# Performance work log

Hardware: AMD Instinct MI355X
Metric: run time of the kernel (lower is better)

## Reference

```python
import jax, jax.numpy as jnp
import numpy as np

NU, NI, ED, H = 30000, 10000, 64, 4
D = ED * H            # fusion_dim = 256
N = NU + NI           # total graph nodes
E = 100000            # edges
B = 8192              # scored (user, wine) pairs
NST, SD = 4, 64       # side tokens / side token dim
NEG = -1e30


def setup_inputs():
    key = jax.random.key(0)
    ks = iter(jax.random.split(key, 64))

    def w(*shape):
        return jax.random.normal(next(ks), shape, jnp.float32) * 0.05

    return {
        "user": jax.random.randint(next(ks), (B,), 0, NU),
        "wine": jax.random.randint(next(ks), (B,), 0, NI),
        "edge_index": jax.random.randint(next(ks), (2, E), 0, N),
        "keep_edge": jax.random.uniform(next(ks), (E,)) > 0.2,   # edge_dropout keep mask
        "node_mask": jax.random.uniform(next(ks), (N,)) < 0.2,   # mask-autoencoding mask
        "user_emb": w(NU, ED),
        "wine_emb": w(NI, ED),
        "up_w": w(ED, D), "up_b": w(D),
        "wp_w": w(ED, D), "wp_b": w(D),
        "sf_proj_w": w(SD, D), "sf_proj_b": w(D),
        "sf_q_w": w(D, D), "sf_q_b": w(D),
        "sf_k_w": w(D, D), "sf_k_b": w(D),
        "sf_v_w": w(D, D), "sf_v_b": w(D),
        "sf_o_w": w(D, D), "sf_o_b": w(D),
        "sf_fc_w": w(2 * D, D), "sf_fc_b": w(D),
        "g_w": w(D, D), "g_b": w(D),
        "t_q_w": w(D, H * D), "t_q_b": w(H * D),
        "t_k_w": w(D, H * D), "t_k_b": w(H * D),
        "t_v_w": w(D, H * D), "t_v_b": w(H * D),
        "t_skip_w": w(D, D), "t_skip_b": w(D),
        "fc_w": w(2 * D, 1), "fc_b": w(1),
        "ae_w": w(D, D), "ae_b": w(D),
        "ep_w": w(2 * D, 1), "ep_b": w(1),
        "wine_side_features": jax.random.normal(next(ks), (NI, NST, SD), jnp.float32),
    }


def _forward(user, wine, edge_index, keep_edge, node_mask,
             user_emb, wine_emb, up_w, up_b, wp_w, wp_b,
             sf_proj_w, sf_proj_b, sf_q_w, sf_q_b, sf_k_w, sf_k_b,
             sf_v_w, sf_v_b, sf_o_w, sf_o_b, sf_fc_w, sf_fc_b,
             g_w, g_b, t_q_w, t_q_b, t_k_w, t_k_b, t_v_w, t_v_b,
             t_skip_w, t_skip_b, fc_w, fc_b, ae_w, ae_b, ep_w, ep_b,
             wine_side_features):
    u_proj = user_emb @ up_w + up_b                       # [NU, D]
    w_proj = wine_emb @ wp_w + wp_b                       # [NI, D]

    # WineSideFusion: single-head attention of wine embedding over side tokens
    side = wine_side_features @ sf_proj_w + sf_proj_b     # [NI, T, D]
    q = w_proj @ sf_q_w + sf_q_b                          # [NI, D]
    k = side @ sf_k_w + sf_k_b                            # [NI, T, D]
    v = side @ sf_v_w + sf_v_b
    attn = jax.nn.softmax(jnp.einsum('nd,ntd->nt', q, k) / jnp.sqrt(jnp.float32(D)), axis=-1)
    ao = jnp.einsum('nt,ntd->nd', attn, v) @ sf_o_w + sf_o_b
    fused = jnp.concatenate([w_proj, ao], axis=1) @ sf_fc_w + sf_fc_b

    x = jnp.concatenate([u_proj, fused], axis=0)          # [N, D]
    src, dst = edge_index[0], edge_index[1]
    ew = keep_edge.astype(x.dtype)                        # edge dropout as 0/1 weights

    # GCNConv (add self loops, symmetric norm)
    deg = jax.ops.segment_sum(ew, dst, num_segments=N) + 1.0
    dinv = jax.lax.rsqrt(deg)
    norm = dinv[src] * dinv[dst] * ew                     # [E]
    xw = x @ g_w                                          # [N, D]
    agg = jax.ops.segment_sum(xw[src] * norm[:, None], dst, num_segments=N)
    x = agg + xw * (dinv * dinv)[:, None] + g_b

    # TransformerConv(heads=H, concat=False): mean over heads + skip
    qh = (x @ t_q_w + t_q_b).reshape(N, H, D)
    kh = (x @ t_k_w + t_k_b).reshape(N, H, D)
    vh = (x @ t_v_w + t_v_b).reshape(N, H, D)
    logits = jnp.einsum('ehd,ehd->eh', qh[dst], kh[src]) / jnp.sqrt(jnp.float32(D))
    logits = jnp.where(keep_edge[:, None], logits, NEG)
    m = jax.ops.segment_max(logits, dst, num_segments=N)  # [N, H]
    m = jnp.where(m < NEG / 2, 0.0, m)                    # guard empty segments
    e = jnp.exp(logits - m[dst]) * ew[:, None]            # [E, H]
    den = jax.ops.segment_sum(e, dst, num_segments=N)     # [N, H]
    num = jax.ops.segment_sum(e[:, :, None] * vh[src], dst, num_segments=N)  # [N, H, D]
    attn_out = num / jnp.maximum(den, 1e-16)[:, :, None]
    x = attn_out.mean(axis=1) + x @ t_skip_w + t_skip_b   # [N, D]

    # Masked autoencoding: masked rows are zeroed, then autoencoded -> recon = bias
    maskf = node_mask.astype(x.dtype)
    recon = ae_b                                          # 0 @ ae_w + ae_b
    diff = recon[None, :] - x                             # [N, D]
    recon_loss = jnp.sum(maskf[:, None] * diff * diff) / (jnp.sum(maskf) * D)

    u_out = x[user]                                       # [B, D]
    w_out = x[wine + NU]                                  # [B, D]
    pair = jnp.concatenate([u_out, w_out], axis=1)        # [B, 2D]

    edge_score = jax.nn.sigmoid(pair @ ep_w + ep_b)       # [B, 1]
    edge_pred_loss = jnp.mean((edge_score - 1.0) ** 2)

    score = jax.nn.sigmoid((pair @ fc_w + fc_b).squeeze(-1)) * 4.0 + 1.0  # [B]
    return score, recon_loss, edge_pred_loss


def reference(user, wine, edge_index, keep_edge, node_mask,
              user_emb, wine_emb, up_w, up_b, wp_w, wp_b,
              sf_proj_w, sf_proj_b, sf_q_w, sf_q_b, sf_k_w, sf_k_b,
              sf_v_w, sf_v_b, sf_o_w, sf_o_b, sf_fc_w, sf_fc_b,
              g_w, g_b, t_q_w, t_q_b, t_k_w, t_k_b, t_v_w, t_v_b,
              t_skip_w, t_skip_b, fc_w, fc_b, ae_w, ae_b, ep_w, ep_b,
              wine_side_features):
    return _forward(user, wine, edge_index, keep_edge, node_mask,
                    user_emb, wine_emb, up_w, up_b, wp_w, wp_b,
                    sf_proj_w, sf_proj_b, sf_q_w, sf_q_b, sf_k_w, sf_k_b,
                    sf_v_w, sf_v_b, sf_o_w, sf_o_b, sf_fc_w, sf_fc_b,
                    g_w, g_b, t_q_w, t_q_b, t_k_w, t_k_b, t_v_w, t_v_b,
                    t_skip_w, t_skip_b, fc_w, fc_b, ae_w, ae_b, ep_w, ep_b,
                    wine_side_features)
```

## Files before the change

### kernel.cpp

```cpp
#include <hip/hip_runtime.h>
#include <stdint.h>

typedef unsigned short u16;
typedef unsigned char u8;
typedef __attribute__((ext_vector_type(8))) short bf16x8;
typedef __attribute__((ext_vector_type(4))) float f32x4;

#define NU_C 30000
#define NI_C 10000
#define N_C  40000
#define E_C  100000
#define B_C  8192

static __device__ __forceinline__ float bf2f(u16 u) {
    union { unsigned int i; float f; } c; c.i = ((unsigned int)u) << 16; return c.f;
}
static __device__ __forceinline__ u16 f2bf(float f) {
    union { float f; unsigned int i; } c; c.f = f;
    return (u16)((c.i + 0x7FFFu + ((c.i >> 16) & 1u)) >> 16);
}
static __device__ __forceinline__ float wave_sum(float v) {
#pragma unroll
    for (int off = 32; off > 0; off >>= 1) v += __shfl_xor(v, off);
    return v;
}

__global__ void zero_kernel(unsigned int* p, int n) {
    int i = blockIdx.x * 256 + threadIdx.x;
    if (i < n) p[i] = 0u;
}
__global__ void fillval_kernel(float* p, int n, float v) {
    int i = blockIdx.x * 256 + threadIdx.x;
    if (i < n) p[i] = v;
}

__global__ void detect_kernel(const unsigned int* a, int n, int* flag) {
    int i = blockIdx.x * 256 + threadIdx.x;
    if (i >= n) return;
    unsigned int v = a[i];
    int f = 0;
    if (v > 1u) f |= 1;
    if (v != 0u && v != 0x3F800000u) f |= 2;
    if (f) atomicOr(flag, f);
}
__global__ void conv_masks_kernel(const void* keep_raw, const void* nm_raw,
                                  u8* km, u8* nm, int E, int N, const int* flag)
{
    int i = blockIdx.x * 256 + threadIdx.x;
    const int f = *flag;
    if (i < E) {
        u8 r;
        if ((f & 1) == 0)      r = ((const int*)keep_raw)[i] != 0;
        else if ((f & 2) == 0) r = ((const float*)keep_raw)[i] != 0.f;
        else                   r = ((const u8*)keep_raw)[i] != 0;
        km[i] = r;
    }
    int j = i - E;
    if (j >= 0 && j < N) {
        u8 r;
        if ((f & 1) == 0)      r = ((const int*)nm_raw)[j] != 0;
        else if ((f & 2) == 0) r = ((const float*)nm_raw)[j] != 0.f;
        else                   r = ((const u8*)nm_raw)[j] != 0;
        nm[j] = r;
    }
}

__global__ void conv3_kernel(const float* __restrict__ a, int na4,
                             const float* __restrict__ b, int nb4,
                             const float* __restrict__ c, int nc4,
                             u16* __restrict__ oa, u16* __restrict__ ob, u16* __restrict__ oc)
{
    int tot = na4 + nb4 + nc4;
    for (int i = blockIdx.x * 256 + threadIdx.x; i < tot; i += gridDim.x * 256) {
        const float* s; u16* o; int j = i;
        if (j < na4) { s = a; o = oa; }
        else if ((j -= na4) < nb4) { s = b; o = ob; }
        else { j -= nb4; s = c; o = oc; }
        float4 v = *(const float4*)&s[(size_t)j * 4];
        ushort4 r;
        r.x = f2bf(v.x); r.y = f2bf(v.y); r.z = f2bf(v.z); r.w = f2bf(v.w);
        *(ushort4*)&o[(size_t)j * 4] = r;
    }
}

#define WT_ELEMS 1359872
__device__ const int wd_prefix[23] = {0,16384,32768,49152,114688,180224,245760,311296,442368,
    507904,573440,638976,704512,770048,835584,901120,966656,1032192,1097728,1163264,1228800,
    1294336,1359872};
__device__ const u8  wd_src[22]  = {0,1,2,3,4,5,6,7,8,9,10,11,12,10,11,12,10,11,12,10,11,12};
__device__ const short wd_ldw[22]= {256,256,256,256,256,256,256,256,256,256,
    1024,1024,1024,1024,1024,1024,1024,1024,1024,1024,1024,1024};
__device__ const short wd_coff[22]={0,0,0,0,0,0,0,0,0,0, 0,0,0, 256,256,256, 512,512,512, 768,768,768};
__device__ const short wd_kmask[22]={63,63,63,255,255,255,255,511,255,255,
    255,255,255,255,255,255,255,255,255,255,255,255};
__device__ const u8  wd_ksh[22] = {6,6,6,8,8,8,8,9,8,8, 8,8,8,8,8,8,8,8,8,8,8,8};

__global__ __launch_bounds__(256)
void wtrans_kernel(const float* w0, const float* w1, const float* w2, const float* w3,
                   const float* w4, const float* w5, const float* w6, const float* w7,
                   const float* w8, const float* w9, const float* w10, const float* w11,
                   const float* w12, u16* __restrict__ WT)
{
    int idx = blockIdx.x * 256 + threadIdx.x;
    if (idx >= WT_ELEMS) return;
    int d = 0;
    while (wd_prefix[d + 1] <= idx) ++d;
    const int local = idx - wd_prefix[d];
    const int k = local & wd_kmask[d];
    const int n = local >> wd_ksh[d];
    const float* s;
    switch (wd_src[d]) {
        case 0: s = w0; break; case 1: s = w1; break; case 2: s = w2; break;
        case 3: s = w3; break; case 4: s = w4; break; case 5: s = w5; break;
        case 6: s = w6; break; case 7: s = w7; break; case 8: s = w8; break;
        case 9: s = w9; break; case 10: s = w10; break; case 11: s = w11; break;
        default: s = w12; break;
    }
    WT[idx] = f2bf(s[(size_t)k * wd_ldw[d] + wd_coff[d] + n]);
}

__global__ void prep_bias_kernel(const float* sfk_b, const float* sfv_b,
                                 const float* tq_b, const float* tk_b, const float* tv_b,
                                 float* kvb, float* qkvb)
{
    int i = blockIdx.x * 256 + threadIdx.x;
    if (i < 512) kvb[i] = i < 256 ? sfk_b[i] : sfv_b[i - 256];
    if (i < 3072) {
        int h = i / 768, j = i - h * 768;
        qkvb[i] = j < 256 ? tq_b[h * 256 + j]
                : (j < 512 ? tk_b[h * 256 + j - 256] : tv_b[h * 256 + j - 512]);
    }
}

template <typename OT>
__global__ __launch_bounds__(512)
void mgemm_kernel(const u16* __restrict__ A, int lda,
                  const u16* __restrict__ WT,
                  const float* __restrict__ bias,
                  OT* __restrict__ C, int ldc,
                  int M, int N, int K)
{
    __shared__ __align__(16) u16 As[256][72];
    __shared__ __align__(16) u16 Bs[128][72];
    const int t = threadIdx.x;
    const int wid = t >> 6, lane = t & 63;
    const int wr = wid >> 1, wc = wid & 1;
    const int lr = lane & 15, lg = lane >> 4;
    const int gx = gridDim.x;
    const int nwg = gx * gridDim.y;
    const int orig = blockIdx.y * gx + blockIdx.x;
    const int q8 = nwg >> 3, r8 = nwg & 7;
    const int xcd = orig & 7, oidx = orig >> 3;
    const int swzb = (xcd < r8 ? xcd * (q8 + 1) : r8 * (q8 + 1) + (xcd - r8) * q8) + oidx;
    const int row0 = (swzb / gx) * 256, col0 = (swzb % gx) * 128;
    const int sra = t >> 1, sha = (t & 1) * 32;
    const int srb = t >> 2, shb = (t & 3) * 16;
    const bool avalid = (row0 + sra) < M;
    const u16* aptr = &A[(size_t)min(row0 + sra, M - 1) * lda];
    const u16* bptr = &WT[(size_t)(col0 + srb) * K];
    const bf16x8 z = {0, 0, 0, 0, 0, 0, 0, 0};
    f32x4 acc[4][4] = {};
    bf16x8 ra[4], rb[2];

    auto gload = [&](int k0) {
#pragma unroll
        for (int j = 0; j < 4; ++j)
            ra[j] = avalid ? *(const bf16x8*)&aptr[k0 + sha + j * 8] : z;
#pragma unroll
        for (int j = 0; j < 2; ++j)
            rb[j] = *(const bf16x8*)&bptr[k0 + shb + j * 8];
    };
    auto swrite = [&]() {
#pragma unroll
        for (int j = 0; j < 4; ++j)
            *(bf16x8*)&As[sra][sha + j * 8] = ra[j];
#pragma unroll
        for (int j = 0; j < 2; ++j)
            *(bf16x8*)&Bs[srb][shb + j * 8] = rb[j];
    };
    auto compute = [&]() {
#pragma unroll
        for (int kk = 0; kk < 2; ++kk) {
            bf16x8 af[4], bfr[4];
#pragma unroll
            for (int m = 0; m < 4; ++m)
                af[m] = *(const bf16x8*)&As[wr * 64 + m * 16 + lr][kk * 32 + lg * 8];
#pragma unroll
            for (int n = 0; n < 4; ++n)
                bfr[n] = *(const bf16x8*)&Bs[wc * 64 + n * 16 + lr][kk * 32 + lg * 8];
#pragma unroll
            for (int m = 0; m < 4; ++m)
#pragma unroll
                for (int n = 0; n < 4; ++n)
                    acc[m][n] = __builtin_amdgcn_mfma_f32_16x16x32_bf16(af[m], bfr[n], acc[m][n], 0, 0, 0);
        }
    };

    gload(0);
    swrite();
    __syncthreads();
    for (int k0 = 64; k0 < K; k0 += 64) {
        gload(k0);
        compute();
        __syncthreads();
        swrite();
        __syncthreads();
    }
    compute();

#pragma unroll
    for (int m = 0; m < 4; ++m) {
#pragma unroll
        for (int r = 0; r < 4; ++r) {
            int row = row0 + wr * 64 + m * 16 + lg * 4 + r;
            if (row >= M) continue;
#pragma unroll
            for (int n = 0; n < 4; ++n) {
                int col = col0 + wc * 64 + n * 16 + lr;
                float v = acc[m][n][r];
                if (bias) v += bias[col];
                if constexpr (sizeof(OT) == 4) C[(size_t)row * ldc + col] = v;
                else C[(size_t)row * ldc + col] = f2bf(v);
            }
        }
    }
}

__global__ __launch_bounds__(256)
void side_attn_kernel(const u16* __restrict__ q, const u16* __restrict__ kv,
                      u16* __restrict__ ao, int NI)
{
    const int wid = threadIdx.x >> 6, lane = threadIdx.x & 63;
    const int n = blockIdx.x * 4 + wid;
    if (n >= NI) return;
    const ushort4 qu = *(const ushort4*)&q[(size_t)n * 256 + lane * 4];
    const float q0 = bf2f(qu.x), q1 = bf2f(qu.y), q2 = bf2f(qu.z), q3 = bf2f(qu.w);
    float logit[4];
#pragma unroll
    for (int tk = 0; tk < 4; ++tk) {
        const ushort4 ku = *(const ushort4*)&kv[((size_t)n * 4 + tk) * 512 + lane * 4];
        float p = q0 * bf2f(ku.x) + q1 * bf2f(ku.y) + q2 * bf2f(ku.z) + q3 * bf2f(ku.w);
        logit[tk] = wave_sum(p) * (1.f / 16.f);
    }
    float mx = fmaxf(fmaxf(logit[0], logit[1]), fmaxf(logit[2], logit[3]));
    float e[4], den = 0.f;
#pragma unroll
    for (int tk = 0; tk < 4; ++tk) { e[tk] = __expf(logit[tk] - mx); den += e[tk]; }
    const float inv = 1.f / den;
    float o0 = 0.f, o1 = 0.f, o2 = 0.f, o3 = 0.f;
#pragma unroll
    for (int tk = 0; tk < 4; ++tk) {
        const ushort4 vu = *(const ushort4*)&kv[((size_t)n * 4 + tk) * 512 + 256 + lane * 4];
        const float w = e[tk] * inv;
        o0 = fmaf(w, bf2f(vu.x), o0); o1 = fmaf(w, bf2f(vu.y), o1);
        o2 = fmaf(w, bf2f(vu.z), o2); o3 = fmaf(w, bf2f(vu.w), o3);
    }
    ushort4 o;
    o.x = f2bf(o0); o.y = f2bf(o1); o.z = f2bf(o2); o.w = f2bf(o3);
    *(ushort4*)&ao[(size_t)n * 256 + lane * 4] = o;
}

__global__ void count_kernel(const int* __restrict__ dst, const u8* __restrict__ keep,
                             int* __restrict__ cnt, float* __restrict__ degw, int E)
{
    int e = blockIdx.x * 256 + threadIdx.x;
    if (e >= E) return;
    int d = dst[e];
    atomicAdd(&cnt[d], 1);
    if (keep[e]) atomicAdd(&degw[d], 1.f);
}

__global__ void dinv_kernel(const float* __restrict__ degw, float* __restrict__ dinv, int N)
{
    int n = blockIdx.x * 256 + threadIdx.x;
    if (n < N) dinv[n] = rsqrtf(degw[n] + 1.f);
}

__global__ __launch_bounds__(1024)
void scan_kernel(const int* __restrict__ cnt, int* __restrict__ rs, int n)
{
    __shared__ int wsum[17];
    __shared__ int s_run;
    const int t = threadIdx.x, lane = t & 63, wid = t >> 6;
    if (t == 0) s_run = 0;
    __syncthreads();
    for (int base = 0; base < n; base += 1024) {
        int i = base + t;
        int v = (i < n) ? cnt[i] : 0;
        int x = v;
#pragma unroll
        for (int off = 1; off < 64; off <<= 1) {
            int y = __shfl_up(x, off);
            if (lane >= off) x += y;
        }
        if (lane == 63) wsum[wid] = x;
        __syncthreads();
        if (t == 0) {
            int a = 0;
            for (int j = 0; j < 16; ++j) { int tmp = wsum[j]; wsum[j] = a; a += tmp; }
            wsum[16] = a;
        }
        __syncthreads();
        if (i < n) rs[i] = s_run + wsum[wid] + x - v;
        __syncthreads();
        if (t == 0) s_run += wsum[16];
        __syncthreads();
    }
    if (t == 0) rs[n] = s_run;
}

__global__ void fill_kernel(const int* __restrict__ dst, const int* __restrict__ rs,
                            int* __restrict__ cursor, int* __restrict__ eid, int E)
{
    int e = blockIdx.x * 256 + threadIdx.x;
    if (e >= E) return;
    int d = dst[e];
    int p = atomicAdd(&cursor[d], 1);
    eid[rs[d] + p] = e;
}

__global__ void sort_kernel(const int* __restrict__ rs, int* __restrict__ eid, int N)
{
    int n = blockIdx.x * 256 + threadIdx.x;
    if (n >= N) return;
    const int b = rs[n], len = rs[n + 1] - b;
    for (int i = 1; i < len; ++i) {
        int key = eid[b + i];
        int j = i - 1;
        while (j >= 0 && eid[b + j] > key) { eid[b + j + 1] = eid[b + j]; --j; }
        eid[b + j + 1] = key;
    }
}

__global__ void edge_prep_kernel(const int* __restrict__ eid, const int* __restrict__ src,
                                 const int* __restrict__ dst, const u8* __restrict__ keep,
                                 const float* __restrict__ dinv,
                                 int* __restrict__ ssrc, float* __restrict__ wnorm, int E)
{
    int i = blockIdx.x * 256 + threadIdx.x;
    if (i >= E) return;
    const int e = eid[i];
    const int s = src[e];
    const u8 k = keep[e];
    ssrc[i] = s * 2 + (int)k;
    wnorm[i] = k ? dinv[s] * dinv[dst[e]] : 0.f;
}

__global__ __launch_bounds__(256)
void gcn_kernel(const u16* __restrict__ xw, const int* __restrict__ ssrc,
                const float* __restrict__ wnorm, const int* __restrict__ rs,
                const float* __restrict__ dinv, const float* __restrict__ gb,
                u16* __restrict__ xout, int N)
{
    const int wid = threadIdx.x >> 6, lane = threadIdx.x & 63;
    const int n = blockIdx.x * 4 + wid;
    if (n >= N) return;
    const float di = dinv[n];
    const float dii = di * di;
    const ushort4 own = *(const ushort4*)&xw[(size_t)n * 256 + lane * 4];
    float a0 = bf2f(own.x) * dii, a1 = bf2f(own.y) * dii;
    float a2 = bf2f(own.z) * dii, a3 = bf2f(own.w) * dii;
    const int e0 = rs[n], e1 = rs[n + 1];
    for (int i = e0; i < e1; ++i) {
        const float w = wnorm[i];
        const int s = ssrc[i] >> 1;
        const ushort4 r = *(const ushort4*)&xw[(size_t)s * 256 + lane * 4];
        a0 = fmaf(bf2f(r.x), w, a0); a1 = fmaf(bf2f(r.y), w, a1);
        a2 = fmaf(bf2f(r.z), w, a2); a3 = fmaf(bf2f(r.w), w, a3);
    }
    const float4 g = *(const float4*)&gb[lane * 4];
    ushort4 o;
    o.x = f2bf(a0 + g.x); o.y = f2bf(a1 + g.y);
    o.z = f2bf(a2 + g.z); o.w = f2bf(a3 + g.w);
    *(ushort4*)&xout[(size_t)n * 256 + lane * 4] = o;
}

__global__ __launch_bounds__(256)
void tconv_head_kernel(const u16* __restrict__ qkv, const int* __restrict__ ssrc,
                       const int* __restrict__ rs, float* __restrict__ xacc, int N)
{
    const int wid = threadIdx.x >> 6, lane = threadIdx.x & 63;
    const int n = blockIdx.x * 4 + wid;
    if (n >= N) return;
    const ushort4 qu = *(const ushort4*)&qkv[(size_t)n * 768 + lane * 4];
    const float q0 = bf2f(qu.x), q1 = bf2f(qu.y), q2 = bf2f(qu.z), q3 = bf2f(qu.w);
    const int e0 = rs[n], e1 = rs[n + 1];
    float m = -1e30f, den = 0.f;
    float a0 = 0.f, a1 = 0.f, a2 = 0.f, a3 = 0.f;
    int i = e0;
    for (; i + 1 < e1; i += 2) {
        const int va = ssrc[i], vb = ssrc[i + 1];
        const int sa = va >> 1, sb = vb >> 1;
        const float ewa = (float)(va & 1), ewb = (float)(vb & 1);
        const ushort4 ka = *(const ushort4*)&qkv[(size_t)sa * 768 + 256 + lane * 4];
        const ushort4 kb = *(const ushort4*)&qkv[(size_t)sb * 768 + 256 + lane * 4];
        const ushort4 xa = *(const ushort4*)&qkv[(size_t)sa * 768 + 512 + lane * 4];
        const ushort4 xb4 = *(const ushort4*)&qkv[(size_t)sb * 768 + 512 + lane * 4];
        float pa = q0 * bf2f(ka.x) + q1 * bf2f(ka.y) + q2 * bf2f(ka.z) + q3 * bf2f(ka.w);
        float pb = q0 * bf2f(kb.x) + q1 * bf2f(kb.y) + q2 * bf2f(kb.z) + q3 * bf2f(kb.w);
        pa = wave_sum(pa) * (1.f / 16.f);
        pb = wave_sum(pb) * (1.f / 16.f);
        {
            const float mn = fmaxf(m, pa);
            const float sc = __expf(m - mn);
            const float w = __expf(pa - mn) * ewa;
            den = den * sc + w;
            a0 = fmaf(w, bf2f(xa.x), a0 * sc); a1 = fmaf(w, bf2f(xa.y), a1 * sc);
            a2 = fmaf(w, bf2f(xa.z), a2 * sc); a3 = fmaf(w, bf2f(xa.w), a3 * sc);
            m = mn;
        }
        {
            const float mn = fmaxf(m, pb);
            const float sc = __expf(m - mn);
            const float w = __expf(pb - mn) * ewb;
            den = den * sc + w;
            a0 = fmaf(w, bf2f(xb4.x), a0 * sc); a1 = fmaf(w, bf2f(xb4.y), a1 * sc);
            a2 = fmaf(w, bf2f(xb4.z), a2 * sc); a3 = fmaf(w, bf2f(xb4.w), a3 * sc);
            m = mn;
        }
    }
    if (i < e1) {
        const int va = ssrc[i];
        const int sa = va >> 1;
        const float ewa = (float)(va & 1);
        const ushort4 ka = *(const ushort4*)&qkv[(size_t)sa * 768 + 256 + lane * 4];
        const ushort4 xa = *(const ushort4*)&qkv[(size_t)sa * 768 + 512 + lane * 4];
        float pa = q0 * bf2f(ka.x) + q1 * bf2f(ka.y) + q2 * bf2f(ka.z) + q3 * bf2f(ka.w);
        pa = wave_sum(pa) * (1.f / 16.f);
        const float mn = fmaxf(m, pa);
        const float sc = __expf(m - mn);
        const float w = __expf(pa - mn) * ewa;
        den = den * sc + w;
        a0 = fmaf(w, bf2f(xa.x), a0 * sc); a1 = fmaf(w, bf2f(xa.y), a1 * sc);
        a2 = fmaf(w, bf2f(xa.z), a2 * sc); a3 = fmaf(w, bf2f(xa.w), a3 * sc);
    }
    const float inv = 0.25f / fmaxf(den, 1e-16f);
    float4* p4 = (float4*)&xacc[(size_t)n * 256 + lane * 4];
    float4 cur = *p4;
    cur.x += a0 * inv; cur.y += a1 * inv; cur.z += a2 * inv; cur.w += a3 * inv;
    *p4 = cur;
}

__global__ __launch_bounds__(256)
void recon_kernel(const float* __restrict__ x, const u8* __restrict__ mask,
                  const float* __restrict__ aeb,
                  float* __restrict__ rblkS, float* __restrict__ rblkC, int N)
{
    const int total = N * 256;
    float s = 0.f, c = 0.f;
    for (int idx = blockIdx.x * 256 + threadIdx.x; idx < total; idx += gridDim.x * 256) {
        const int n = idx >> 8, d = idx & 255;
        if (mask[n]) {
            const float diff = aeb[d] - x[idx];
            s = fmaf(diff, diff, s);
            if (d == 0) c += 1.f;
        }
    }
    s = wave_sum(s); c = wave_sum(c);
    __shared__ float ss[4], cc[4];
    const int lane = threadIdx.x & 63, wid = threadIdx.x >> 6;
    if (lane == 0) { ss[wid] = s; cc[wid] = c; }
    __syncthreads();
    if (threadIdx.x == 0) {
        rblkS[blockIdx.x] = ss[0] + ss[1] + ss[2] + ss[3];
        rblkC[blockIdx.x] = cc[0] + cc[1] + cc[2] + cc[3];
    }
}

__global__ __launch_bounds__(256)
void score_kernel(const float* __restrict__ x, const int* __restrict__ user,
                  const int* __restrict__ wine,
                  const float* __restrict__ epw, const float* __restrict__ epb,
                  const float* __restrict__ fcw, const float* __restrict__ fcb,
                  float* __restrict__ out, float* __restrict__ sblk, int B)
{
    __shared__ float sep[4];
    const int wid = threadIdx.x >> 6, lane = threadIdx.x & 63;
    const int b = blockIdx.x * 4 + wid;
    if (b < B) {
        const size_t u = (size_t)user[b];
        const size_t w = (size_t)wine[b] + NU_C;
        const float4 xu = *(const float4*)&x[u * 256 + lane * 4];
        const float4 xw = *(const float4*)&x[w * 256 + lane * 4];
        const float4 e1 = *(const float4*)&epw[lane * 4];
        const float4 e2 = *(const float4*)&epw[256 + lane * 4];
        const float4 f1 = *(const float4*)&fcw[lane * 4];
        const float4 f2 = *(const float4*)&fcw[256 + lane * 4];
        float pep = xu.x * e1.x + xu.y * e1.y + xu.z * e1.z + xu.w * e1.w
                  + xw.x * e2.x + xw.y * e2.y + xw.z * e2.z + xw.w * e2.w;
        float pfc = xu.x * f1.x + xu.y * f1.y + xu.z * f1.z + xu.w * f1.w
                  + xw.x * f2.x + xw.y * f2.y + xw.z * f2.z + xw.w * f2.w;
        pep = wave_sum(pep); pfc = wave_sum(pfc);
        if (lane == 0) {
            const float es = 1.f / (1.f + __expf(-(pep + epb[0])));
            sep[wid] = (es - 1.f) * (es - 1.f);
            out[b] = 1.f / (1.f + __expf(-(pfc + fcb[0]))) * 4.f + 1.f;
        }
    } else if (lane == 0) {
        sep[wid] = 0.f;
    }
    __syncthreads();
    if (threadIdx.x == 0) sblk[blockIdx.x] = sep[0] + sep[1] + sep[2] + sep[3];
}

__global__ __launch_bounds__(1024)
void final_reduce_kernel(const float* __restrict__ rblkS, const float* __restrict__ rblkC,
                         const float* __restrict__ sblk, float* __restrict__ out, int B)
{
    const int t = threadIdx.x, lane = t & 63, wid = t >> 6;
    float s = rblkS[t] + rblkS[t + 1024];
    float c = rblkC[t] + rblkC[t + 1024];
    float p = sblk[t] + sblk[t + 1024];
    s = wave_sum(s); c = wave_sum(c); p = wave_sum(p);
    __shared__ float ss[16], cc[16], pp[16];
    if (lane == 0) { ss[wid] = s; cc[wid] = c; pp[wid] = p; }
    __syncthreads();
    if (t == 0) {
        float S = 0.f, C = 0.f, P = 0.f;
        for (int i = 0; i < 16; ++i) { S += ss[i]; C += cc[i]; P += pp[i]; }
        out[B] = S / (C * 256.f);
        out[B + 1] = P / (float)B;
    }
}

extern "C" void kernel_launch(void* const* d_in, const int* in_sizes, int n_in,
                              void* d_out, int out_size, void* d_ws, size_t ws_size,
                              hipStream_t stream)
{
    const int* user = (const int*)d_in[0];
    const int* wine = (const int*)d_in[1];
    const int* e_src = (const int*)d_in[2];
    const int* e_dst = e_src + E_C;
    const void* keep_raw  = d_in[3];
    const void* nmask_raw = d_in[4];
    const float* user_emb = (const float*)d_in[5];
    const float* wine_emb = (const float*)d_in[6];
    const float* up_w = (const float*)d_in[7];
    const float* up_b = (const float*)d_in[8];
    const float* wp_w = (const float*)d_in[9];
    const float* wp_b = (const float*)d_in[10];
    const float* sf_proj_w = (const float*)d_in[11];
    const float* sf_proj_b = (const float*)d_in[12];
    const float* sf_q_w = (const float*)d_in[13];
    const float* sf_q_b = (const float*)d_in[14];
    const float* sf_k_w = (const float*)d_in[15];
    const float* sf_k_b = (const float*)d_in[16];
    const float* sf_v_w = (const float*)d_in[17];
    const float* sf_v_b = (const float*)d_in[18];
    const float* sf_o_w = (const float*)d_in[19];
    const float* sf_o_b = (const float*)d_in[20];
    const float* sf_fc_w = (const float*)d_in[21];
    const float* sf_fc_b = (const float*)d_in[22];
    const float* g_w = (const float*)d_in[23];
    const float* g_b = (const float*)d_in[24];
    const float* t_q_w = (const float*)d_in[25];
    const float* t_q_b = (const float*)d_in[26];
    const float* t_k_w = (const float*)d_in[27];
    const float* t_k_b = (const float*)d_in[28];
    const float* t_v_w = (const float*)d_in[29];
    const float* t_v_b = (const float*)d_in[30];
    const float* t_skip_w = (const float*)d_in[31];
    const float* t_skip_b = (const float*)d_in[32];
    const float* fc_w = (const float*)d_in[33];
    const float* fc_b = (const float*)d_in[34];
    const float* ae_b = (const float*)d_in[36];
    const float* ep_w = (const float*)d_in[37];
    const float* ep_b = (const float*)d_in[38];
    const float* wsf = (const float*)d_in[39];
    float* out = (float*)d_out;
    char* ws = (char*)d_ws;

    size_t off = 0;
    auto take = [&](size_t b) { size_t r = off; off += (b + 255) & ~(size_t)255; return r; };
    const size_t o_xb     = take((size_t)N_C * 256 * 2);
    const size_t o_cnt    = take((size_t)N_C * 4);
    const size_t o_degw   = take((size_t)N_C * 4);
    const size_t o_cursor = take((size_t)N_C * 4);
    const size_t o_scal   = take(256);
    const size_t o_rowst  = take((size_t)(N_C + 1) * 4);
    const size_t o_dinv   = take((size_t)N_C * 4);
    const size_t o_eid    = take((size_t)E_C * 4);
    const size_t o_ssrc   = take((size_t)E_C * 4);
    const size_t o_wnorm  = take((size_t)E_C * 4);
    const size_t o_kmask  = take((size_t)E_C);
    const size_t o_nmask  = take((size_t)N_C);
    const size_t o_rblkS  = take(2048 * 4);
    const size_t o_rblkC  = take(2048 * 4);
    const size_t o_sblk   = take(2048 * 4);
    const size_t o_wt     = take((size_t)WT_ELEMS * 2);
    const size_t o_bias   = take(3584 * 4);
    const size_t ARENA    = 102400000;
    const size_t o_arena  = take(ARENA);
    const size_t NEED = off;

    if (ws_size < NEED) {
        fillval_kernel<<<dim3((out_size + 255) / 256), 256, 0, stream>>>(
            out, out_size, (float)((double)ws_size / (1024.0 * 1024.0)));
        return;
    }

    u16*   xb     = (u16*)  (ws + o_xb);
    int*   cnt    = (int*)  (ws + o_cnt);
    float* degw   = (float*)(ws + o_degw);
    int*   cursor = (int*)  (ws + o_cursor);
    int*   flag   = (int*)  (ws + o_scal);
    int*   rowst  = (int*)  (ws + o_rowst);
    float* dinvb  = (float*)(ws + o_dinv);
    int*   eid    = (int*)  (ws + o_eid);
    int*   ssrc   = (int*)  (ws + o_ssrc);
    float* wnorm  = (float*)(ws + o_wnorm);
    u8*    kmask  = (u8*)   (ws + o_kmask);
    u8*    nmaskb = (u8*)   (ws + o_nmask);
    float* rblkS  = (float*)(ws + o_rblkS);
    float* rblkC  = (float*)(ws + o_rblkC);
    float* sblk   = (float*)(ws + o_sblk);
    u16*   WT     = (u16*)  (ws + o_wt);
    float* kvb    = (float*)(ws + o_bias);
    float* qkvb   = kvb + 512;

    u16* wt_up   = WT + 0;
    u16* wt_wp   = WT + 16384;
    u16* wt_proj = WT + 32768;
    u16* wt_sfq  = WT + 49152;
    u16* wt_sfkv = WT + 114688;
    u16* wt_sfo  = WT + 245760;
    u16* wt_sffc = WT + 311296;
    u16* wt_g    = WT + 442368;
    u16* wt_skip = WT + 507904;
    u16* wt_qkv  = WT + 573440;

    u16* ue16  = (u16*)(ws + o_arena);
    u16* we16  = (u16*)(ws + o_arena + 3840000);
    u16* wsf16 = (u16*)(ws + o_arena + 5120000);
    u16* cat   = (u16*)(ws + o_arena + 10240000);
    u16* side  = (u16*)(ws + o_arena + 20480000);
    u16* qbuf  = (u16*)(ws + o_arena + 40960000);
    u16* kvbuf = (u16*)(ws + o_arena + 46080000);
    u16* aobuf = (u16*)(ws + o_arena + 87040000);
    u16* xw    = (u16*)(ws + o_arena);
    u16* qkvh  = (u16*)(ws + o_arena);
    float* xacc = (float*)(ws + o_arena + 61440000);

    const int zero_words = (3 * N_C * 4 + 256) / 4;
    zero_kernel<<<dim3((zero_words + 255) / 256), 256, 0, stream>>>((unsigned int*)cnt, zero_words);

    detect_kernel<<<dim3((E_C / 4 + 255) / 256), 256, 0, stream>>>((const unsigned int*)keep_raw, E_C / 4, flag);
    conv_masks_kernel<<<dim3((E_C + N_C + 255) / 256), 256, 0, stream>>>(keep_raw, nmask_raw, kmask, nmaskb, E_C, N_C, flag);

    conv3_kernel<<<dim3(2048), 256, 0, stream>>>(user_emb, NU_C * 16, wine_emb, NI_C * 16,
                                                 wsf, N_C * 16, ue16, we16, wsf16);
    wtrans_kernel<<<dim3(WT_ELEMS / 256), 256, 0, stream>>>(up_w, wp_w, sf_proj_w, sf_q_w,
        sf_k_w, sf_v_w, sf_o_w, sf_fc_w, g_w, t_skip_w, t_q_w, t_k_w, t_v_w, WT);
    prep_bias_kernel<<<dim3(12), 256, 0, stream>>>(sf_k_b, sf_v_b, t_q_b, t_k_b, t_v_b, kvb, qkvb);

    mgemm_kernel<u16><<<dim3(2, 118), 512, 0, stream>>>(ue16, 64, wt_up, up_b, xb, 256, NU_C, 256, 64);
    mgemm_kernel<u16><<<dim3(2, 40), 512, 0, stream>>>(we16, 64, wt_wp, wp_b, cat, 512, NI_C, 256, 64);
    mgemm_kernel<u16><<<dim3(2, 157), 512, 0, stream>>>(wsf16, 64, wt_proj, sf_proj_b, side, 256, N_C, 256, 64);
    mgemm_kernel<u16><<<dim3(2, 40), 512, 0, stream>>>(cat, 512, wt_sfq, sf_q_b, qbuf, 256, NI_C, 256, 256);
    mgemm_kernel<u16><<<dim3(4, 157), 512, 0, stream>>>(side, 256, wt_sfkv, kvb, kvbuf, 512, N_C, 512, 256);
    side_attn_kernel<<<dim3(2500), 256, 0, stream>>>(qbuf, kvbuf, aobuf, NI_C);
    mgemm_kernel<u16><<<dim3(2, 40), 512, 0, stream>>>(aobuf, 256, wt_sfo, sf_o_b, cat + 256, 512, NI_C, 256, 256);
    mgemm_kernel<u16><<<dim3(2, 40), 512, 0, stream>>>(cat, 512, wt_sffc, sf_fc_b, xb + (size_t)NU_C * 256, 256, NI_C, 256, 512);

    count_kernel<<<dim3((E_C + 255) / 256), 256, 0, stream>>>(e_dst, kmask, cnt, degw, E_C);
    dinv_kernel<<<dim3((N_C + 255) / 256), 256, 0, stream>>>(degw, dinvb, N_C);
    scan_kernel<<<dim3(1), 1024, 0, stream>>>(cnt, rowst, N_C);
    fill_kernel<<<dim3((E_C + 255) / 256), 256, 0, stream>>>(e_dst, rowst, cursor, eid, E_C);
    sort_kernel<<<dim3((N_C + 255) / 256), 256, 0, stream>>>(rowst, eid, N_C);
    edge_prep_kernel<<<dim3((E_C + 255) / 256), 256, 0, stream>>>(eid, e_src, e_dst, kmask, dinvb, ssrc, wnorm, E_C);

    mgemm_kernel<u16><<<dim3(2, 157), 512, 0, stream>>>(xb, 256, wt_g, nullptr, xw, 256, N_C, 256, 256);
    gcn_kernel<<<dim3(N_C / 4), 256, 0, stream>>>(xw, ssrc, wnorm, rowst, dinvb, g_b, xb, N_C);

    mgemm_kernel<float><<<dim3(2, 157), 512, 0, stream>>>(xb, 256, wt_skip, t_skip_b, xacc, 256, N_C, 256, 256);
    for (int h = 0; h < 4; ++h) {
        mgemm_kernel<u16><<<dim3(6, 157), 512, 0, stream>>>(xb, 256, wt_qkv + h * 196608,
                                                            qkvb + h * 768, qkvh, 768, N_C, 768, 256);
        tconv_head_kernel<<<dim3(N_C / 4), 256, 0, stream>>>(qkvh, ssrc, rowst, xacc, N_C);
    }

    recon_kernel<<<dim3(2048), 256, 0, stream>>>(xacc, nmaskb, ae_b, rblkS, rblkC, N_C);
    score_kernel<<<dim3(2048), 256, 0, stream>>>(xacc, user, wine, ep_w, ep_b, fc_w, fc_b, out, sblk, B_C);
    final_reduce_kernel<<<dim3(1), 1024, 0, stream>>>(rblkS, rblkC, sblk, out, B_C);
}
```

Baseline: 604.5 us.

## Process four nodes per wave in transformer-conv head with 16-lane groups

The attention head kernel now maps 16 lanes to each destination node instead of a full 64-lane wave, so each wave handles four nodes. Each lane loads 16 bf16 values with vector loads and the dot product is reduced with a 4-step 16-lane shuffle instead of a 6-step full-wave reduction. The grid shrinks by a factor of four. The GCN aggregation loop is also unrolled by two edges to overlap gathers. Register pressure rises from 16 accumulators per lane, and lanes in a wave may diverge when the four nodes have different degrees.

Result: no change. 610.6 us (+1.0%).

```diff
diff --git a/kernel.cpp b/kernel.cpp
--- a/kernel.cpp
+++ b/kernel.cpp
@@ -23,6 +23,20 @@
 #pragma unroll
     for (int off = 32; off > 0; off >>= 1) v += __shfl_xor(v, off);
     return v;
+}
+static __device__ __forceinline__ float group_sum16(float v) {
+#pragma unroll
+    for (int off = 8; off > 0; off >>= 1) v += __shfl_xor(v, off);
+    return v;
+}
+static __device__ __forceinline__ float dot16(const bf16x8 a0, const bf16x8 a1,
+                                              const bf16x8 b0, const bf16x8 b1) {
+    float p = 0.f;
+#pragma unroll
+    for (int j = 0; j < 8; ++j) p = fmaf(bf2f((u16)a0[j]), bf2f((u16)b0[j]), p);
+#pragma unroll
+    for (int j = 0; j < 8; ++j) p = fmaf(bf2f((u16)a1[j]), bf2f((u16)b1[j]), p);
+    return p;
 }
 
 __global__ void zero_kernel(unsigned int* p, int n) {
@@ -361,12 +375,23 @@
     float a0 = bf2f(own.x) * dii, a1 = bf2f(own.y) * dii;
     float a2 = bf2f(own.z) * dii, a3 = bf2f(own.w) * dii;
     const int e0 = rs[n], e1 = rs[n + 1];
-    for (int i = e0; i < e1; ++i) {
-        const float w = wnorm[i];
-        const int s = ssrc[i] >> 1;
-        const ushort4 r = *(const ushort4*)&xw[(size_t)s * 256 + lane * 4];
-        a0 = fmaf(bf2f(r.x), w, a0); a1 = fmaf(bf2f(r.y), w, a1);
-        a2 = fmaf(bf2f(r.z), w, a2); a3 = fmaf(bf2f(r.w), w, a3);
+    int i = e0;
+    for (; i + 1 < e1; i += 2) {
+        const float wa = wnorm[i], wb = wnorm[i + 1];
+        const int sa = ssrc[i] >> 1, sb = ssrc[i + 1] >> 1;
+        const ushort4 ra = *(const ushort4*)&xw[(size_t)sa * 256 + lane * 4];
+        const ushort4 rb = *(const ushort4*)&xw[(size_t)sb * 256 + lane * 4];
+        a0 = fmaf(bf2f(rb.x), wb, fmaf(bf2f(ra.x), wa, a0));
+        a1 = fmaf(bf2f(rb.y), wb, fmaf(bf2f(ra.y), wa, a1));
+        a2 = fmaf(bf2f(rb.z), wb, fmaf(bf2f(ra.z), wa, a2));
+        a3 = fmaf(bf2f(rb.w), wb, fmaf(bf2f(ra.w), wa, a3));
+    }
+    if (i < e1) {
+        const float wa = wnorm[i];
+        const int sa = ssrc[i] >> 1;
+        const ushort4 r = *(const ushort4*)&xw[(size_t)sa * 256 + lane * 4];
+        a0 = fmaf(bf2f(r.x), wa, a0); a1 = fmaf(bf2f(r.y), wa, a1);
+        a2 = fmaf(bf2f(r.z), wa, a2); a3 = fmaf(bf2f(r.w), wa, a3);
     }
     const float4 g = *(const float4*)&gb[lane * 4];
     ushort4 o;
@@ -380,33 +405,38 @@
                        const int* __restrict__ rs, float* __restrict__ xacc, int N)
 {
     const int wid = threadIdx.x >> 6, lane = threadIdx.x & 63;
-    const int n = blockIdx.x * 4 + wid;
+    const int g = lane >> 4, s = lane & 15;
+    const int n = blockIdx.x * 16 + wid * 4 + g;
     if (n >= N) return;
-    const ushort4 qu = *(const ushort4*)&qkv[(size_t)n * 768 + lane * 4];
-    const float q0 = bf2f(qu.x), q1 = bf2f(qu.y), q2 = bf2f(qu.z), q3 = bf2f(qu.w);
+    const bf16x8 qa = *(const bf16x8*)&qkv[(size_t)n * 768 + s * 16];
+    const bf16x8 qb = *(const bf16x8*)&qkv[(size_t)n * 768 + s * 16 + 8];
     const int e0 = rs[n], e1 = rs[n + 1];
     float m = -1e30f, den = 0.f;
-    float a0 = 0.f, a1 = 0.f, a2 = 0.f, a3 = 0.f;
+    float ac[16] = {};
     int i = e0;
     for (; i + 1 < e1; i += 2) {
         const int va = ssrc[i], vb = ssrc[i + 1];
-        const int sa = va >> 1, sb = vb >> 1;
+        const size_t sa = (size_t)(va >> 1) * 768, sb = (size_t)(vb >> 1) * 768;
         const float ewa = (float)(va & 1), ewb = (float)(vb & 1);
-        const ushort4 ka = *(const ushort4*)&qkv[(size_t)sa * 768 + 256 + lane * 4];
-        const ushort4 kb = *(const ushort4*)&qkv[(size_t)sb * 768 + 256 + lane * 4];
-        const ushort4 xa = *(const ushort4*)&qkv[(size_t)sa * 768 + 512 + lane * 4];
-        const ushort4 xb4 = *(const ushort4*)&qkv[(size_t)sb * 768 + 512 + lane * 4];
-        float pa = q0 * bf2f(ka.x) + q1 * bf2f(ka.y) + q2 * bf2f(ka.z) + q3 * bf2f(ka.w);
-        float pb = q0 * bf2f(kb.x) + q1 * bf2f(kb.y) + q2 * bf2f(kb.z) + q3 * bf2f(kb.w);
-        pa = wave_sum(pa) * (1.f / 16.f);
-        pb = wave_sum(pb) * (1.f / 16.f);
+        const bf16x8 ka0 = *(const bf16x8*)&qkv[sa + 256 + s * 16];
+        const bf16x8 ka1 = *(const bf16x8*)&qkv[sa + 256 + s * 16 + 8];
+        const bf16x8 kb0 = *(const bf16x8*)&qkv[sb + 256 + s * 16];
+        const bf16x8 kb1 = *(const bf16x8*)&qkv[sb + 256 + s * 16 + 8];
+        const bf16x8 xa0 = *(const bf16x8*)&qkv[sa + 512 + s * 16];
+        const bf16x8 xa1 = *(const bf16x8*)&qkv[sa + 512 + s * 16 + 8];
+        const bf16x8 xb0 = *(const bf16x8*)&qkv[sb + 512 + s * 16];
+        const bf16x8 xb1 = *(const bf16x8*)&qkv[sb + 512 + s * 16 + 8];
+        float pa = group_sum16(dot16(qa, qb, ka0, ka1)) * (1.f / 16.f);
+        float pb = group_sum16(dot16(qa, qb, kb0, kb1)) * (1.f / 16.f);
         {
             const float mn = fmaxf(m, pa);
             const float sc = __expf(m - mn);
             const float w = __expf(pa - mn) * ewa;
             den = den * sc + w;
-            a0 = fmaf(w, bf2f(xa.x), a0 * sc); a1 = fmaf(w, bf2f(xa.y), a1 * sc);
-            a2 = fmaf(w, bf2f(xa.z), a2 * sc); a3 = fmaf(w, bf2f(xa.w), a3 * sc);
+#pragma unroll
+            for (int j = 0; j < 8; ++j) ac[j] = fmaf(w, bf2f((u16)xa0[j]), ac[j] * sc);
+#pragma unroll
+            for (int j = 0; j < 8; ++j) ac[8 + j] = fmaf(w, bf2f((u16)xa1[j]), ac[8 + j] * sc);
             m = mn;
         }
         {
@@ -414,31 +444,40 @@
             const float sc = __expf(m - mn);
             const float w = __expf(pb - mn) * ewb;
             den = den * sc + w;
-            a0 = fmaf(w, bf2f(xb4.x), a0 * sc); a1 = fmaf(w, bf2f(xb4.y), a1 * sc);
-            a2 = fmaf(w, bf2f(xb4.z), a2 * sc); a3 = fmaf(w, bf2f(xb4.w), a3 * sc);
+#pragma unroll
+            for (int j = 0; j < 8; ++j) ac[j] = fmaf(w, bf2f((u16)xb0[j]), ac[j] * sc);
+#pragma unroll
+            for (int j = 0; j < 8; ++j) ac[8 + j] = fmaf(w, bf2f((u16)xb1[j]), ac[8 + j] * sc);
             m = mn;
         }
     }
     if (i < e1) {
         const int va = ssrc[i];
-        const int sa = va >> 1;
+        const size_t sa = (size_t)(va >> 1) * 768;
         const float ewa = (float)(va & 1);
-        const ushort4 ka = *(const ushort4*)&qkv[(size_t)sa * 768 + 256 + lane * 4];
-        const ushort4 xa = *(const ushort4*)&qkv[(size_t)sa * 768 + 512 + lane * 4];
-        float pa = q0 * bf2f(ka.x) + q1 * bf2f(ka.y) + q2 * bf2f(ka.z) + q3 * bf2f(ka.w);
-        pa = wave_sum(pa) * (1.f / 16.f);
+        const bf16x8 ka0 = *(const bf16x8*)&qkv[sa + 256 + s * 16];
+        const bf16x8 ka1 = *(const bf16x8*)&qkv[sa + 256 + s * 16 + 8];
+        const bf16x8 xa0 = *(const bf16x8*)&qkv[sa + 512 + s * 16];
+        const bf16x8 xa1 = *(const bf16x8*)&qkv[sa + 512 + s * 16 + 8];
+        float pa = group_sum16(dot16(qa, qb, ka0, ka1)) * (1.f / 16.f);
         const float mn = fmaxf(m, pa);
         const float sc = __expf(m - mn);
         const float w = __expf(pa - mn) * ewa;
         den = den * sc + w;
-        a0 = fmaf(w, bf2f(xa.x), a0 * sc); a1 = fmaf(w, bf2f(xa.y), a1 * sc);
-        a2 = fmaf(w, bf2f(xa.z), a2 * sc); a3 = fmaf(w, bf2f(xa.w), a3 * sc);
+#pragma unroll
+        for (int j = 0; j < 8; ++j) ac[j] = fmaf(w, bf2f((u16)xa0[j]), ac[j] * sc);
+#pragma unroll
+        for (int j = 0; j < 8; ++j) ac[8 + j] = fmaf(w, bf2f((u16)xa1[j]), ac[8 + j] * sc);
     }
     const float inv = 0.25f / fmaxf(den, 1e-16f);
-    float4* p4 = (float4*)&xacc[(size_t)n * 256 + lane * 4];
-    float4 cur = *p4;
-    cur.x += a0 * inv; cur.y += a1 * inv; cur.z += a2 * inv; cur.w += a3 * inv;
-    *p4 = cur;
+    float4* p4 = (float4*)&xacc[(size_t)n * 256 + s * 16];
+#pragma unroll
+    for (int q = 0; q < 4; ++q) {
+        float4 cur = p4[q];
+        cur.x += ac[q * 4 + 0] * inv; cur.y += ac[q * 4 + 1] * inv;
+        cur.z += ac[q * 4 + 2] * inv; cur.w += ac[q * 4 + 3] * inv;
+        p4[q] = cur;
+    }
 }
 
 __global__ __launch_bounds__(256)
@@ -676,7 +715,7 @@
     for (int h = 0; h < 4; ++h) {
         mgemm_kernel<u16><<<dim3(6, 157), 512, 0, stream>>>(xb, 256, wt_qkv + h * 196608,
                                                             qkvb + h * 768, qkvh, 768, N_C, 768, 256);
-        tconv_head_kernel<<<dim3(N_C / 4), 256, 0, stream>>>(qkvh, ssrc, rowst, xacc, N_C);
+        tconv_head_kernel<<<dim3(N_C / 16), 256, 0, stream>>>(qkvh, ssrc, rowst, xacc, N_C);
     }
 
     recon_kernel<<<dim3(2048), 256, 0, stream>>>(xacc, nmaskb, ae_b, rblkS, rblkC, N_C);
```
